# Kernel tuning notes

Measured on AMD Instinct MI355X. Metric: run time of the kernel, lower is better.

The kernel has to match this reference:

```python
import jax, jax.numpy as jnp
import numpy as np

N_NODES = 65536
N_EDGES = 524288
IN_CH = 128
FHC = 256      # first_hc = max(hidden, in)
HID = 256
NCLS = 3
NODES_PER_GRAPH = 32


def setup_inputs() -> dict:
    key = jax.random.key(0)
    ks = jax.random.split(key, 16)
    s = 1.0 / np.sqrt(FHC)
    inp = {
        "x": jax.random.normal(ks[0], (N_NODES, IN_CH), dtype=jnp.float32),
        "edge_index": jax.random.randint(ks[1], (2, N_EDGES), 0, N_NODES, dtype=jnp.int64),
        "edge_attr": jax.random.uniform(ks[2], (N_EDGES,), dtype=jnp.float32),
        # GatedGraphConv params: per-layer matmul weight + GRUCell
        "gg_w": jax.random.uniform(ks[3], (2, FHC, FHC), minval=-s, maxval=s, dtype=jnp.float32),
        "w_ih": jax.random.uniform(ks[4], (3 * FHC, FHC), minval=-s, maxval=s, dtype=jnp.float32),
        "w_hh": jax.random.uniform(ks[5], (3 * FHC, FHC), minval=-s, maxval=s, dtype=jnp.float32),
        "b_ih": jax.random.uniform(ks[6], (3 * FHC,), minval=-s, maxval=s, dtype=jnp.float32),
        "b_hh": jax.random.uniform(ks[7], (3 * FHC,), minval=-s, maxval=s, dtype=jnp.float32),
        # Conv1d(FHC, 1, kernel_size=1)
        "cnn_w": jax.random.uniform(ks[8], (1, FHC, 1), minval=-s, maxval=s, dtype=jnp.float32),
        "cnn_b": jax.random.uniform(ks[9], (1,), minval=-s, maxval=s, dtype=jnp.float32),
        # Linear(32, HID), Linear(HID, NCLS)
        "lin1_w": jax.random.uniform(ks[10], (HID, NODES_PER_GRAPH), minval=-0.17, maxval=0.17, dtype=jnp.float32),
        "lin1_b": jax.random.uniform(ks[11], (HID,), minval=-0.17, maxval=0.17, dtype=jnp.float32),
        "lin2_w": jax.random.uniform(ks[12], (NCLS, HID), minval=-s, maxval=s, dtype=jnp.float32),
        "lin2_b": jax.random.uniform(ks[13], (NCLS,), minval=-s, maxval=s, dtype=jnp.float32),
    }
    return inp


def _gated_graph_conv(x, src, dst, edge_w, gg_w, w_ih, w_hh, b_ih, b_hh):
    # PyG GatedGraphConv: pad input to out_channels, then num_layers iterations.
    n = x.shape[0]
    h = jnp.pad(x, ((0, 0), (0, FHC - x.shape[1])))  # [N, FHC]
    for i in range(2):
        m = h @ gg_w[i]                                   # [N, FHC]
        msgs = m[src] * edge_w[:, None]                   # gather per edge [E, FHC]
        agg = jax.ops.segment_sum(msgs, dst, num_segments=n)  # scatter-add [N, FHC]
        # GRUCell(input=agg, hidden=h), torch gate order: r, z, n
        gi = agg @ w_ih.T + b_ih
        gh = h @ w_hh.T + b_hh
        ir, iz, ig = jnp.split(gi, 3, axis=1)
        hr, hz, hg = jnp.split(gh, 3, axis=1)
        r = jax.nn.sigmoid(ir + hr)
        z = jax.nn.sigmoid(iz + hz)
        g = jnp.tanh(ig + r * hg)
        h = (1.0 - z) * g + z * h
    return h


def reference(x, edge_index, edge_attr, gg_w, w_ih, w_hh, b_ih, b_hh,
              cnn_w, cnn_b, lin1_w, lin1_b, lin2_w, lin2_b):
    src, dst = edge_index[0], edge_index[1]
    h = _gated_graph_conv(x, src, dst, edge_attr, gg_w, w_ih, w_hh, b_ih, b_hh)
    h = jax.nn.relu(h)  # dropout is identity in eval mode
    bs = h.shape[0] // NODES_PER_GRAPH
    h = h.reshape(bs, NODES_PER_GRAPH, FHC)          # (bs e) f -> bs e f
    # Conv1d(FHC,1,k=1) over layout (bs, f, e): y[b,e] = sum_f w[0,f,0]*h[b,e,f] + b
    y = jnp.einsum('bef,f->be', h, cnn_w[:, :, 0].reshape(FHC)) + cnn_b[0]
    y = jax.nn.relu(y)                               # [bs, 32]
    y = y @ lin1_w.T + lin1_b
    y = jax.nn.relu(y)
    y = y @ lin2_w.T + lin2_b
    return jax.nn.softmax(y, axis=-1)
```

## Files before the change

kernel.cpp:

```cpp
#include <hip/hip_runtime.h>
#include <math.h>

#define N_NODES 65536
#define N_EDGES 524288
#define IN_CH 128
#define FHC 256
#define NCLS 3
#define NPG 32
#define NGRAPH (N_NODES / NPG)

typedef __attribute__((ext_vector_type(8))) short bfrag;
typedef __attribute__((ext_vector_type(4))) float facc;

__device__ __forceinline__ float fast_sigmoid(float x) {
    return __builtin_amdgcn_rcpf(1.0f + __expf(-x));
}
__device__ __forceinline__ float fast_tanh(float x) {
    return 1.0f - 2.0f * __builtin_amdgcn_rcpf(__expf(2.0f * x) + 1.0f);
}

__device__ inline short f2bf(float f) {
    union { float f; unsigned u; } v; v.f = f;
    unsigned r = v.u + 0x7fffu + ((v.u >> 16) & 1u);
    return (short)(r >> 16);
}
__device__ inline float bf2f(short s) {
    union { unsigned u; float f; } v; v.u = ((unsigned)(unsigned short)s) << 16;
    return v.f;
}

__device__ __forceinline__ void gld16(const short* g, short* l) {
    __builtin_amdgcn_global_load_lds(
        (const __attribute__((address_space(1))) void*)g,
        (__attribute__((address_space(3))) void*)l, 16, 0, 0);
}

template <int N> __device__ __forceinline__ void vwait() {
    if constexpr (N == 0)       asm volatile("s_waitcnt vmcnt(0)" ::: "memory");
    else if constexpr (N == 2)  asm volatile("s_waitcnt vmcnt(2)" ::: "memory");
    else if constexpr (N == 4)  asm volatile("s_waitcnt vmcnt(4)" ::: "memory");
    else if constexpr (N == 6)  asm volatile("s_waitcnt vmcnt(6)" ::: "memory");
    else if constexpr (N == 8)  asm volatile("s_waitcnt vmcnt(8)" ::: "memory");
    else if constexpr (N == 10) asm volatile("s_waitcnt vmcnt(10)" ::: "memory");
    else                        asm volatile("s_waitcnt vmcnt(12)" ::: "memory");
}

__global__ void prep_kernel(const float* __restrict__ gg_w, const float* __restrict__ wih,
                            const float* __restrict__ whh, const float* __restrict__ x,
                            short* __restrict__ gg16, short* __restrict__ wih16,
                            short* __restrict__ whh16, short* __restrict__ h) {
    int bid = blockIdx.x;
    if (bid < 2048) {
        int t = bid * 256 + threadIdx.x;
        if (t < 2 * FHC * FHC) {
            gg16[t] = f2bf(gg_w[t]);
        } else if (t < 5 * FHC * FHC) {
            int u = t - 2 * FHC * FHC;
            wih16[u] = f2bf(wih[u]);
        } else {
            int u = t - 5 * FHC * FHC;
            whh16[u] = f2bf(whh[u]);
        }
    } else {
        int idx = (bid - 2048) * 256 + threadIdx.x;
        int c4 = idx & 63, n = idx >> 6;
        short4 v = {0, 0, 0, 0};
        if (c4 < 32) {
            float4 xv = reinterpret_cast<const float4*>(x)[n * 32 + c4];
            v.x = f2bf(xv.x); v.y = f2bf(xv.y); v.z = f2bf(xv.z); v.w = f2bf(xv.w);
        }
        reinterpret_cast<short4*>(h)[idx] = v;
    }
}

__global__ void hist_kernel(const int* __restrict__ ei, int* __restrict__ deg) {
    int e = blockIdx.x * 256 + threadIdx.x;
    atomicAdd(&deg[ei[N_EDGES + e]], 1);
}

__global__ void scan_reduce_kernel(const int* __restrict__ deg, int* __restrict__ bsum) {
    __shared__ int s[256];
    int t = threadIdx.x;
    s[t] = deg[blockIdx.x * 256 + t];
    __syncthreads();
    for (int off = 128; off > 0; off >>= 1) {
        if (t < off) s[t] += s[t + off];
        __syncthreads();
    }
    if (t == 0) bsum[blockIdx.x] = s[0];
}

__global__ void scan_write_kernel(const int* __restrict__ deg, const int* __restrict__ bsum,
                                  int* __restrict__ rowptr, int* __restrict__ cur) {
    __shared__ int s[256];
    __shared__ int s2[256];
    int t = threadIdx.x, gid = blockIdx.x * 256 + t;
    int v = deg[gid];
    s[t] = v;
    int bv = bsum[t];
    s2[t] = bv;
    __syncthreads();
    for (int off = 1; off < 256; off <<= 1) {
        int u = (t >= off) ? s[t - off] : 0;
        int u2 = (t >= off) ? s2[t - off] : 0;
        __syncthreads();
        s[t] += u;
        s2[t] += u2;
        __syncthreads();
    }
    int boff = s2[blockIdx.x] - bsum[blockIdx.x];
    int excl = boff + s[t] - v;
    rowptr[gid] = excl;
    cur[gid] = excl;
    if (gid == N_NODES - 1) rowptr[N_NODES] = excl + v;
}

__global__ void fill_kernel(const int* __restrict__ ei, const float* __restrict__ ea,
                            int* __restrict__ cur, int2* __restrict__ csr) {
    int e = blockIdx.x * 256 + threadIdx.x;
    int dst = ei[N_EDGES + e];
    int pos = atomicAdd(&cur[dst], 1);
    csr[pos] = make_int2(ei[e], __float_as_int(ea[e]));
}

__global__ __launch_bounds__(256) void gather_kernel(const short* __restrict__ m,
                                                     const int* __restrict__ rowptr,
                                                     const int2* __restrict__ csr,
                                                     short* __restrict__ agg16) {
    int node = blockIdx.x * 4 + (threadIdx.x >> 6);
    int lane = threadIdx.x & 63;
    int beg = rowptr[node], end = rowptr[node + 1];
    const short4* m4 = reinterpret_cast<const short4*>(m);
    float a0 = 0.f, a1 = 0.f, a2 = 0.f, a3 = 0.f;
#define GSTEP(E)                                            \
    {                                                       \
        float w = __int_as_float((E).y);                    \
        short4 v = m4[(size_t)(E).x * 64 + lane];           \
        a0 += bf2f(v.x) * w;                                \
        a1 += bf2f(v.y) * w;                                \
        a2 += bf2f(v.z) * w;                                \
        a3 += bf2f(v.w) * w;                                \
    }
    int j = beg;
    for (; j + 8 <= end; j += 8) {
        int2 e0 = csr[j + 0], e1 = csr[j + 1], e2 = csr[j + 2], e3 = csr[j + 3];
        int2 e4 = csr[j + 4], e5 = csr[j + 5], e6 = csr[j + 6], e7 = csr[j + 7];
        GSTEP(e0) GSTEP(e1) GSTEP(e2) GSTEP(e3)
        GSTEP(e4) GSTEP(e5) GSTEP(e6) GSTEP(e7)
    }
    for (; j + 2 <= end; j += 2) {
        int2 e0 = csr[j + 0], e1 = csr[j + 1];
        GSTEP(e0) GSTEP(e1)
    }
    if (j < end) {
        int2 e0 = csr[j];
        GSTEP(e0)
    }
#undef GSTEP
    short4 o;
    o.x = f2bf(a0); o.y = f2bf(a1); o.z = f2bf(a2); o.w = f2bf(a3);
    reinterpret_cast<short4*>(agg16)[(size_t)node * 64 + lane] = o;
}

__global__ __launch_bounds__(256, 2) void mgemm_kernel(const short* __restrict__ A,
                                                       const short* __restrict__ Wbase,
                                                       short* __restrict__ Cbase) {
    __shared__ __align__(16) short lds[3 * 16 * 512];
    int tid = threadIdx.x;
    int lane = tid & 63, wv = tid >> 6, fr = lane & 15, fc = lane >> 4;
    int sel = blockIdx.y >> 1;
    const short* W = Wbase + (size_t)sel * FHC * FHC;
    short* C = Cbase + (size_t)sel * 3 * FHC * FHC;
    int m0 = blockIdx.x * 128, n0 = (blockIdx.y & 1) * 128;
    int srow = lane >> 2;
    int scol = (lane & 3) ^ ((lane >> 3) & 3);
    const short* gsrc[4];
    int ldsoff[4];
#pragma unroll
    for (int i = 0; i < 4; ++i) {
        int ch = wv * 4 + i;
        if (ch < 8) {
            ldsoff[i] = ch * 512;
            gsrc[i] = A + (size_t)(m0 + ch * 16 + srow) * FHC + scol * 8;
        } else {
            ldsoff[i] = 4096 + (ch - 8) * 512;
            gsrc[i] = W + (size_t)(n0 + (ch - 8) * 16 + srow) * FHC + scol * 8;
        }
    }
    int fcs = fc ^ ((fr >> 1) & 3);

    auto STAGE = [&](int ks, int bufsel) {
        short* dst = &lds[bufsel * 8192];
#pragma unroll
        for (int i = 0; i < 4; ++i) gld16(gsrc[i] + ks * 32, dst + ldsoff[i]);
    };

    facc acc[2][8] = {};
    STAGE(0, 0);
    STAGE(1, 1);
    for (int ks = 0; ks < 8; ++ks) {
        if (ks < 7) { asm volatile("s_waitcnt vmcnt(4)" ::: "memory"); }
        else        { asm volatile("s_waitcnt vmcnt(0)" ::: "memory"); }
        __builtin_amdgcn_sched_barrier(0);
        __builtin_amdgcn_s_barrier();
        __builtin_amdgcn_sched_barrier(0);
        if (ks + 2 < 8) STAGE(ks + 2, (ks + 2) % 3);
        __builtin_amdgcn_sched_barrier(0);
        const short* B = &lds[(ks % 3) * 8192];
        int ar = (wv * 32 + fr) * 32 + fcs * 8;
        bfrag a0 = *reinterpret_cast<const bfrag*>(B + ar);
        bfrag a1 = *reinterpret_cast<const bfrag*>(B + ar + 16 * 32);
        __builtin_amdgcn_s_setprio(1);
#pragma unroll
        for (int cf = 0; cf < 8; ++cf) {
            bfrag b = *reinterpret_cast<const bfrag*>(B + 4096 + (cf * 16 + fr) * 32 + fcs * 8);
            acc[0][cf] = __builtin_amdgcn_mfma_f32_16x16x32_bf16(a0, b, acc[0][cf], 0, 0, 0);
            acc[1][cf] = __builtin_amdgcn_mfma_f32_16x16x32_bf16(a1, b, acc[1][cf], 0, 0, 0);
        }
        __builtin_amdgcn_s_setprio(0);
    }
#pragma unroll
    for (int s = 0; s < 2; ++s)
#pragma unroll
        for (int cf = 0; cf < 8; ++cf)
#pragma unroll
            for (int r = 0; r < 4; ++r) {
                int node = m0 + wv * 32 + s * 16 + fc * 4 + r;
                int c = n0 + cf * 16 + fr;
                C[(size_t)node * FHC + c] = f2bf(acc[s][cf][r]);
            }
}

template <int NKS>
__global__ __launch_bounds__(256, 2) void gru_fused_kernel(
    const short* __restrict__ hagg16, const short* __restrict__ hin, short* __restrict__ hout,
    const short* __restrict__ wfT, const short* __restrict__ whh16,
    const float* __restrict__ bih, const float* __restrict__ bhh) {
    constexpr int NCH = 2 * NKS;
    constexpr int NL = NCH / 4;
    constexpr int BUF = NCH * 512;
    __shared__ __align__(16) short lds[3 * BUF];
    int tid = threadIdx.x;
    int lane = tid & 63, wv = tid >> 6, fr = lane & 15, fc = lane >> 4;
    int c = blockIdx.y * 64 + wv * 16 + fr;

    bfrag wreg[6][NKS];
    {
        size_t roff = (size_t)c * FHC + fc * 8;
#pragma unroll
        for (int ks = 0; ks < NKS; ++ks) {
            wreg[0][ks] = *reinterpret_cast<const bfrag*>(wfT + roff + ks * 32);
            wreg[1][ks] = *reinterpret_cast<const bfrag*>(wfT + (size_t)256 * FHC + roff + ks * 32);
            wreg[2][ks] = *reinterpret_cast<const bfrag*>(wfT + (size_t)512 * FHC + roff + ks * 32);
            wreg[3][ks] = *reinterpret_cast<const bfrag*>(whh16 + roff + ks * 32);
            wreg[4][ks] = *reinterpret_cast<const bfrag*>(whh16 + (size_t)256 * FHC + roff + ks * 32);
            wreg[5][ks] = *reinterpret_cast<const bfrag*>(whh16 + (size_t)512 * FHC + roff + ks * 32);
        }
    }
    float br = bih[c] + bhh[c];
    float bz = bih[c + 256] + bhh[c + 256];
    float big = bih[c + 512], bhg = bhh[c + 512];

    int srow = lane >> 2;
    int scol = (lane & 3) ^ ((lane >> 3) & 3);
    const short* gb[NL];
    int ldsoff[NL];
#pragma unroll
    for (int i = 0; i < NL; ++i) {
        int ch = wv * NL + i;
        int ks = ch & (NKS - 1);
        const short* src = (ch >= NKS) ? hin : hagg16;
        gb[i] = src + (size_t)srow * FHC + ks * 32 + scol * 8;
        ldsoff[i] = ch * 512;
    }
    int fcs = fc ^ ((fr >> 1) & 3);
    int lo = (fr * 4 + fcs) * 8;
    const int NT = 32;
    int tile0 = blockIdx.x * NT;

    int cc = (NKS == 4 && c >= 128) ? 0 : c;
    int hbase = (NKS + (cc >> 5)) * 512 + (cc & 7);
    int hg = (cc >> 3) & 3;
    bool hvalid = (NKS == 8) || (c < 128);

    auto STAGE = [&](int t, int bufsel) {
        size_t noff = (size_t)(tile0 + t) * 16 * FHC;
        short* dst = &lds[bufsel * BUF];
#pragma unroll
        for (int i = 0; i < NL; ++i) gld16(gb[i] + noff, dst + ldsoff[i]);
    };

    STAGE(0, 0);
    STAGE(1, 1);
    for (int t = 0; t < NT; ++t) {
        if (t == 0)           vwait<NL>();
        else if (t == 1)      vwait<NL + 4>();
        else if (t == NT - 1) vwait<8>();
        else                  vwait<NL + 8>();
        __builtin_amdgcn_sched_barrier(0);
        __builtin_amdgcn_s_barrier();
        __builtin_amdgcn_sched_barrier(0);
        if (t + 2 < NT) STAGE(t + 2, (t + 2) % 3);
        __builtin_amdgcn_sched_barrier(0);
        const short* B = &lds[(t % 3) * BUF];
        facc aR = {}, aZ = {}, aG = {}, aH = {};
        __builtin_amdgcn_s_setprio(1);
#pragma unroll
        for (int ks = 0; ks < NKS; ++ks) {
            bfrag ag = *reinterpret_cast<const bfrag*>(B + ks * 512 + lo);
            bfrag hh = *reinterpret_cast<const bfrag*>(B + (NKS + ks) * 512 + lo);
            aR = __builtin_amdgcn_mfma_f32_16x16x32_bf16(ag, wreg[0][ks], aR, 0, 0, 0);
            aR = __builtin_amdgcn_mfma_f32_16x16x32_bf16(hh, wreg[3][ks], aR, 0, 0, 0);
            aZ = __builtin_amdgcn_mfma_f32_16x16x32_bf16(ag, wreg[1][ks], aZ, 0, 0, 0);
            aZ = __builtin_amdgcn_mfma_f32_16x16x32_bf16(hh, wreg[4][ks], aZ, 0, 0, 0);
            aG = __builtin_amdgcn_mfma_f32_16x16x32_bf16(ag, wreg[2][ks], aG, 0, 0, 0);
            aH = __builtin_amdgcn_mfma_f32_16x16x32_bf16(hh, wreg[5][ks], aH, 0, 0, 0);
        }
        __builtin_amdgcn_s_setprio(0);
        int node0 = (tile0 + t) * 16;
#pragma unroll
        for (int r = 0; r < 4; ++r) {
            int row = fc * 4 + r;
            float hold = hvalid ? bf2f(B[hbase + (row * 4 + (hg ^ ((row >> 1) & 3))) * 8]) : 0.f;
            float rg = fast_sigmoid(aR[r] + br);
            float z = fast_sigmoid(aZ[r] + bz);
            float g = fast_tanh(aG[r] + big + rg * (aH[r] + bhg));
            hout[(size_t)(node0 + row) * FHC + c] = f2bf(g + z * (hold - g));
        }
    }
}

__global__ __launch_bounds__(256) void head_kernel(
    const short* __restrict__ h, const float* __restrict__ cw, const float* __restrict__ cb,
    const float* __restrict__ l1w, const float* __restrict__ l1b,
    const float* __restrict__ l2w, const float* __restrict__ l2b, float* __restrict__ out) {
    __shared__ float ys[32];
    __shared__ float zs[256];
    __shared__ float os[3];
    int b = blockIdx.x, tid = threadIdx.x;
    {
        int node = b * 32 + (tid >> 3);
        int c0 = (tid & 7) * 32;
        const short4* hp = reinterpret_cast<const short4*>(&h[(size_t)node * FHC + c0]);
        float p = 0.f;
#pragma unroll
        for (int q = 0; q < 8; ++q) {
            short4 hv = hp[q];
            const float* wq = &cw[c0 + q * 4];
            p += fmaxf(bf2f(hv.x), 0.f) * wq[0] + fmaxf(bf2f(hv.y), 0.f) * wq[1] +
                 fmaxf(bf2f(hv.z), 0.f) * wq[2] + fmaxf(bf2f(hv.w), 0.f) * wq[3];
        }
        p += __shfl_down(p, 4, 64);
        p += __shfl_down(p, 2, 64);
        p += __shfl_down(p, 1, 64);
        if ((tid & 7) == 0) ys[tid >> 3] = fmaxf(p + cb[0], 0.f);
    }
    __syncthreads();
    float acc = l1b[tid];
#pragma unroll
    for (int k = 0; k < 32; ++k) acc += ys[k] * l1w[tid * 32 + k];
    zs[tid] = fmaxf(acc, 0.f);
    __syncthreads();
    int wave = tid >> 6, lane = tid & 63;
    if (wave < 3) {
        float p = 0.f;
#pragma unroll
        for (int j = 0; j < 4; ++j) p += zs[lane + j * 64] * l2w[wave * 256 + lane + j * 64];
#pragma unroll
        for (int off = 32; off > 0; off >>= 1) p += __shfl_down(p, off, 64);
        if (lane == 0) os[wave] = p + l2b[wave];
    }
    __syncthreads();
    if (tid == 0) {
        float mx = fmaxf(os[0], fmaxf(os[1], os[2]));
        float e0 = expf(os[0] - mx), e1 = expf(os[1] - mx), e2 = expf(os[2] - mx);
        float s = e0 + e1 + e2;
        out[b * 3 + 0] = e0 / s;
        out[b * 3 + 1] = e1 / s;
        out[b * 3 + 2] = e2 / s;
    }
}

extern "C" void kernel_launch(void* const* d_in, const int* in_sizes, int n_in,
                              void* d_out, int out_size, void* d_ws, size_t ws_size,
                              hipStream_t stream) {
    const float* x = (const float*)d_in[0];
    const int* ei = (const int*)d_in[1];
    const float* ea = (const float*)d_in[2];
    const float* gg_w = (const float*)d_in[3];
    const float* w_ih = (const float*)d_in[4];
    const float* w_hh = (const float*)d_in[5];
    const float* b_ih = (const float*)d_in[6];
    const float* b_hh = (const float*)d_in[7];
    const float* cnn_w = (const float*)d_in[8];
    const float* cnn_b = (const float*)d_in[9];
    const float* l1w = (const float*)d_in[10];
    const float* l1b = (const float*)d_in[11];
    const float* l2w = (const float*)d_in[12];
    const float* l2b = (const float*)d_in[13];
    float* out = (float*)d_out;

    const size_t nodeE = (size_t)N_NODES * FHC;
    char* p = (char*)d_ws;
    short* hA = (short*)p;      p += nodeE * 2;
    short* hB = (short*)p;      p += nodeE * 2;
    short* hagg = (short*)p;    p += nodeE * 2;
    short* gg16 = (short*)p;    p += (size_t)2 * FHC * FHC * 2;
    short* wih16 = (short*)p;   p += (size_t)3 * FHC * FHC * 2;
    short* whh16 = (short*)p;   p += (size_t)3 * FHC * FHC * 2;
    short* wfT0 = (short*)p;    p += (size_t)3 * FHC * FHC * 2;
    short* wfT1 = (short*)p;    p += (size_t)3 * FHC * FHC * 2;
    int* deg = (int*)p;         p += (size_t)N_NODES * 4;
    int* rowptr = (int*)p;      p += (size_t)(N_NODES + 4) * 4;
    int* cur = (int*)p;         p += (size_t)N_NODES * 4;
    int* bsum = (int*)p;        p += 256 * 4;
    int2* csr = (int2*)p;       p += (size_t)N_EDGES * 8;
    (void)wfT1;

    dim3 grid_wf(768 / 128, 4);
    dim3 grid_gru(128, 4);

    prep_kernel<<<2048 + N_NODES * 64 / 256, 256, 0, stream>>>(gg_w, w_ih, w_hh, x,
                                                               gg16, wih16, whh16, hA);

    mgemm_kernel<<<grid_wf, 256, 0, stream>>>(wih16, gg16, wfT0);

    hipMemsetAsync(deg, 0, (size_t)N_NODES * 4, stream);
    hist_kernel<<<N_EDGES / 256, 256, 0, stream>>>(ei, deg);
    scan_reduce_kernel<<<N_NODES / 256, 256, 0, stream>>>(deg, bsum);
    scan_write_kernel<<<N_NODES / 256, 256, 0, stream>>>(deg, bsum, rowptr, cur);
    fill_kernel<<<N_EDGES / 256, 256, 0, stream>>>(ei, ea, cur, csr);

    gather_kernel<<<N_NODES / 4, 256, 0, stream>>>(hA, rowptr, csr, hagg);
    gru_fused_kernel<4><<<grid_gru, 256, 0, stream>>>(hagg, hA, hB, wfT0, whh16, b_ih, b_hh);

    gather_kernel<<<N_NODES / 4, 256, 0, stream>>>(hB, rowptr, csr, hagg);
    gru_fused_kernel<8><<<grid_gru, 256, 0, stream>>>(hagg, hB, hA,
                                                      wfT0 + (size_t)3 * FHC * FHC, whh16,
                                                      b_ih, b_hh);

    head_kernel<<<NGRAPH, 256, 0, stream>>>(hA, cnn_w, cnn_b, l1w, l1b, l2w, l2b, out);
}
```

Measured before the change: 265.9 us.

## Split GRU K-reduction across two wave halves with LDS partial-sum exchange

```diff
diff --git a/kernel.cpp b/kernel.cpp
--- a/kernel.cpp
+++ b/kernel.cpp
@@ -36,13 +36,14 @@
 }
 
 template <int N> __device__ __forceinline__ void vwait() {
-    if constexpr (N == 0)       asm volatile("s_waitcnt vmcnt(0)" ::: "memory");
-    else if constexpr (N == 2)  asm volatile("s_waitcnt vmcnt(2)" ::: "memory");
-    else if constexpr (N == 4)  asm volatile("s_waitcnt vmcnt(4)" ::: "memory");
-    else if constexpr (N == 6)  asm volatile("s_waitcnt vmcnt(6)" ::: "memory");
-    else if constexpr (N == 8)  asm volatile("s_waitcnt vmcnt(8)" ::: "memory");
-    else if constexpr (N == 10) asm volatile("s_waitcnt vmcnt(10)" ::: "memory");
-    else                        asm volatile("s_waitcnt vmcnt(12)" ::: "memory");
+    if constexpr (N == 0)      asm volatile("s_waitcnt vmcnt(0)" ::: "memory");
+    else if constexpr (N == 1) asm volatile("s_waitcnt vmcnt(1)" ::: "memory");
+    else if constexpr (N == 2) asm volatile("s_waitcnt vmcnt(2)" ::: "memory");
+    else if constexpr (N == 3) asm volatile("s_waitcnt vmcnt(3)" ::: "memory");
+    else if constexpr (N == 4) asm volatile("s_waitcnt vmcnt(4)" ::: "memory");
+    else if constexpr (N == 5) asm volatile("s_waitcnt vmcnt(5)" ::: "memory");
+    else if constexpr (N == 6) asm volatile("s_waitcnt vmcnt(6)" ::: "memory");
+    else                       asm volatile("s_waitcnt vmcnt(8)" ::: "memory");
 }
 
 __global__ void prep_kernel(const float* __restrict__ gg_w, const float* __restrict__ wih,
@@ -232,29 +233,34 @@
 }
 
 template <int NKS>
-__global__ __launch_bounds__(256, 2) void gru_fused_kernel(
+__global__ __launch_bounds__(512, 2) void gru_fused_kernel(
     const short* __restrict__ hagg16, const short* __restrict__ hin, short* __restrict__ hout,
     const short* __restrict__ wfT, const short* __restrict__ whh16,
     const float* __restrict__ bih, const float* __restrict__ bhh) {
+    constexpr int NKH = NKS / 2;
     constexpr int NCH = 2 * NKS;
-    constexpr int NL = NCH / 4;
+    constexpr int NL = NCH / 8;
     constexpr int BUF = NCH * 512;
-    __shared__ __align__(16) short lds[3 * BUF];
+    __shared__ __align__(16) short lds[3 * BUF + 8192];
+    float* xbuf = reinterpret_cast<float*>(&lds[3 * BUF]);
     int tid = threadIdx.x;
-    int lane = tid & 63, wv = tid >> 6, fr = lane & 15, fc = lane >> 4;
-    int c = blockIdx.y * 64 + wv * 16 + fr;
-
-    bfrag wreg[6][NKS];
+    int lane = tid & 63, wv = tid >> 6;
+    int pair = wv & 3, half = wv >> 2;
+    int fr = lane & 15, fc = lane >> 4;
+    int c = blockIdx.y * 64 + pair * 16 + fr;
+
+    bfrag wreg[6][NKH];
     {
         size_t roff = (size_t)c * FHC + fc * 8;
 #pragma unroll
-        for (int ks = 0; ks < NKS; ++ks) {
-            wreg[0][ks] = *reinterpret_cast<const bfrag*>(wfT + roff + ks * 32);
-            wreg[1][ks] = *reinterpret_cast<const bfrag*>(wfT + (size_t)256 * FHC + roff + ks * 32);
-            wreg[2][ks] = *reinterpret_cast<const bfrag*>(wfT + (size_t)512 * FHC + roff + ks * 32);
-            wreg[3][ks] = *reinterpret_cast<const bfrag*>(whh16 + roff + ks * 32);
-            wreg[4][ks] = *reinterpret_cast<const bfrag*>(whh16 + (size_t)256 * FHC + roff + ks * 32);
-            wreg[5][ks] = *reinterpret_cast<const bfrag*>(whh16 + (size_t)512 * FHC + roff + ks * 32);
+        for (int kk = 0; kk < NKH; ++kk) {
+            int ks = half * NKH + kk;
+            wreg[0][kk] = *reinterpret_cast<const bfrag*>(wfT + roff + ks * 32);
+            wreg[1][kk] = *reinterpret_cast<const bfrag*>(wfT + (size_t)256 * FHC + roff + ks * 32);
+            wreg[2][kk] = *reinterpret_cast<const bfrag*>(wfT + (size_t)512 * FHC + roff + ks * 32);
+            wreg[3][kk] = *reinterpret_cast<const bfrag*>(whh16 + roff + ks * 32);
+            wreg[4][kk] = *reinterpret_cast<const bfrag*>(whh16 + (size_t)256 * FHC + roff + ks * 32);
+            wreg[5][kk] = *reinterpret_cast<const bfrag*>(whh16 + (size_t)512 * FHC + roff + ks * 32);
         }
     }
     float br = bih[c] + bhh[c];
@@ -283,6 +289,10 @@
     int hg = (cc >> 3) & 3;
     bool hvalid = (NKS == 8) || (c < 128);
 
+    float* xw = xbuf + pair * 1024 + half * 512 + lane;
+    const float* xr = xbuf + pair * 1024 + (1 - half) * 512 + lane;
+    int row0 = fc * 4 + half * 2;
+
     auto STAGE = [&](int t, int bufsel) {
         size_t noff = (size_t)(tile0 + t) * 16 * FHC;
         short* dst = &lds[bufsel * BUF];
@@ -294,9 +304,9 @@
     STAGE(1, 1);
     for (int t = 0; t < NT; ++t) {
         if (t == 0)           vwait<NL>();
-        else if (t == 1)      vwait<NL + 4>();
-        else if (t == NT - 1) vwait<8>();
-        else                  vwait<NL + 8>();
+        else if (t == 1)      vwait<NL + 2>();
+        else if (t == NT - 1) vwait<4>();
+        else                  vwait<NL + 4>();
         __builtin_amdgcn_sched_barrier(0);
         __builtin_amdgcn_s_barrier();
         __builtin_amdgcn_sched_barrier(0);
@@ -306,26 +316,54 @@
         facc aR = {}, aZ = {}, aG = {}, aH = {};
         __builtin_amdgcn_s_setprio(1);
 #pragma unroll
-        for (int ks = 0; ks < NKS; ++ks) {
+        for (int kk = 0; kk < NKH; ++kk) {
+            int ks = half * NKH + kk;
             bfrag ag = *reinterpret_cast<const bfrag*>(B + ks * 512 + lo);
             bfrag hh = *reinterpret_cast<const bfrag*>(B + (NKS + ks) * 512 + lo);
-            aR = __builtin_amdgcn_mfma_f32_16x16x32_bf16(ag, wreg[0][ks], aR, 0, 0, 0);
-            aR = __builtin_amdgcn_mfma_f32_16x16x32_bf16(hh, wreg[3][ks], aR, 0, 0, 0);
-            aZ = __builtin_amdgcn_mfma_f32_16x16x32_bf16(ag, wreg[1][ks], aZ, 0, 0, 0);
-            aZ = __builtin_amdgcn_mfma_f32_16x16x32_bf16(hh, wreg[4][ks], aZ, 0, 0, 0);
-            aG = __builtin_amdgcn_mfma_f32_16x16x32_bf16(ag, wreg[2][ks], aG, 0, 0, 0);
-            aH = __builtin_amdgcn_mfma_f32_16x16x32_bf16(hh, wreg[5][ks], aH, 0, 0, 0);
+            aR = __builtin_amdgcn_mfma_f32_16x16x32_bf16(ag, wreg[0][kk], aR, 0, 0, 0);
+            aR = __builtin_amdgcn_mfma_f32_16x16x32_bf16(hh, wreg[3][kk], aR, 0, 0, 0);
+            aZ = __builtin_amdgcn_mfma_f32_16x16x32_bf16(ag, wreg[1][kk], aZ, 0, 0, 0);
+            aZ = __builtin_amdgcn_mfma_f32_16x16x32_bf16(hh, wreg[4][kk], aZ, 0, 0, 0);
+            aG = __builtin_amdgcn_mfma_f32_16x16x32_bf16(ag, wreg[2][kk], aG, 0, 0, 0);
+            aH = __builtin_amdgcn_mfma_f32_16x16x32_bf16(hh, wreg[5][kk], aH, 0, 0, 0);
         }
         __builtin_amdgcn_s_setprio(0);
+        if (half == 0) {
+            xw[0] = aR[2]; xw[64] = aR[3]; xw[128] = aZ[2]; xw[192] = aZ[3];
+            xw[256] = aG[2]; xw[320] = aG[3]; xw[384] = aH[2]; xw[448] = aH[3];
+        } else {
+            xw[0] = aR[0]; xw[64] = aR[1]; xw[128] = aZ[0]; xw[192] = aZ[1];
+            xw[256] = aG[0]; xw[320] = aG[1]; xw[384] = aH[0]; xw[448] = aH[1];
+        }
+        asm volatile("s_waitcnt lgkmcnt(0)" ::: "memory");
+        __builtin_amdgcn_sched_barrier(0);
+        __builtin_amdgcn_s_barrier();
+        __builtin_amdgcn_sched_barrier(0);
+        float p0 = xr[0], p1 = xr[64], p2 = xr[128], p3 = xr[192];
+        float p4 = xr[256], p5 = xr[320], p6 = xr[384], p7 = xr[448];
+        float sR0, sR1, sZ0, sZ1, sG0, sG1, sH0, sH1;
+        if (half == 0) {
+            sR0 = aR[0] + p0; sR1 = aR[1] + p1; sZ0 = aZ[0] + p2; sZ1 = aZ[1] + p3;
+            sG0 = aG[0] + p4; sG1 = aG[1] + p5; sH0 = aH[0] + p6; sH1 = aH[1] + p7;
+        } else {
+            sR0 = aR[2] + p0; sR1 = aR[3] + p1; sZ0 = aZ[2] + p2; sZ1 = aZ[3] + p3;
+            sG0 = aG[2] + p4; sG1 = aG[3] + p5; sH0 = aH[2] + p6; sH1 = aH[3] + p7;
+        }
         int node0 = (tile0 + t) * 16;
-#pragma unroll
-        for (int r = 0; r < 4; ++r) {
-            int row = fc * 4 + r;
-            float hold = hvalid ? bf2f(B[hbase + (row * 4 + (hg ^ ((row >> 1) & 3))) * 8]) : 0.f;
-            float rg = fast_sigmoid(aR[r] + br);
-            float z = fast_sigmoid(aZ[r] + bz);
-            float g = fast_tanh(aG[r] + big + rg * (aH[r] + bhg));
-            hout[(size_t)(node0 + row) * FHC + c] = f2bf(g + z * (hold - g));
+        {
+            float hold = hvalid ? bf2f(B[hbase + (row0 * 4 + (hg ^ ((row0 >> 1) & 3))) * 8]) : 0.f;
+            float rg = fast_sigmoid(sR0 + br);
+            float z = fast_sigmoid(sZ0 + bz);
+            float g = fast_tanh(sG0 + big + rg * (sH0 + bhg));
+            hout[(size_t)(node0 + row0) * FHC + c] = f2bf(g + z * (hold - g));
+        }
+        {
+            int row1 = row0 + 1;
+            float hold = hvalid ? bf2f(B[hbase + (row1 * 4 + (hg ^ ((row1 >> 1) & 3))) * 8]) : 0.f;
+            float rg = fast_sigmoid(sR1 + br);
+            float z = fast_sigmoid(sZ1 + bz);
+            float g = fast_tanh(sG1 + big + rg * (sH1 + bhg));
+            hout[(size_t)(node0 + row1) * FHC + c] = f2bf(g + z * (hold - g));
         }
     }
 }
@@ -432,10 +470,10 @@
     fill_kernel<<<N_EDGES / 256, 256, 0, stream>>>(ei, ea, cur, csr);
 
     gather_kernel<<<N_NODES / 4, 256, 0, stream>>>(hA, rowptr, csr, hagg);
-    gru_fused_kernel<4><<<grid_gru, 256, 0, stream>>>(hagg, hA, hB, wfT0, whh16, b_ih, b_hh);
+    gru_fused_kernel<4><<<grid_gru, 512, 0, stream>>>(hagg, hA, hB, wfT0, whh16, b_ih, b_hh);
 
     gather_kernel<<<N_NODES / 4, 256, 0, stream>>>(hB, rowptr, csr, hagg);
-    gru_fused_kernel<8><<<grid_gru, 256, 0, stream>>>(hagg, hB, hA,
+    gru_fused_kernel<8><<<grid_gru, 512, 0, stream>>>(hagg, hB, hA,
                                                       wfT0 + (size_t)3 * FHC * FHC, whh16,
                                                       b_ih, b_hh);
 
```

Result: slower. 318.2 us (+19.7%).
